# Kernel optimization log

Measured on AMD Instinct MI355X. Metric: run time of the kernel, lower is better.

The kernel has to match this reference:

```python
import jax, jax.numpy as jnp
import numpy as np

N, E, F_IN, H, MH, C, G = 100000, 3200000, 128, 32, 64, 10, 64

def _seg_sum(data, ids, num):
    return jax.ops.segment_sum(data, ids, num_segments=num)

def gcn_conv(x, row, col, ew, W, b, n):
    # PyG GCNConv: linear first, then self-loops + symmetric edge-weight norm + scatter-add
    h = x @ W  # [N, H]
    loop = jnp.arange(n)
    r = jnp.concatenate([row, loop])
    c = jnp.concatenate([col, loop])
    w = jnp.concatenate([ew, jnp.ones((n,), dtype=ew.dtype)])
    deg = _seg_sum(w, c, n)
    dinv = jnp.where(deg > 0, jax.lax.rsqrt(deg), 0.0)
    norm = dinv[r] * w * dinv[c]  # [E+N]
    out = _seg_sum(norm[:, None] * h[r], c, n)  # scatter to targets
    return out + b

def setup_inputs():
    key = jax.random.key(0)
    ks = jax.random.split(key, 16)
    inp = {
        "x": jax.random.normal(ks[0], (N, F_IN), dtype=jnp.float32),
        "edge_index": jax.random.randint(ks[1], (2, E), 0, N, dtype=jnp.int64),
        "edge_weight": jax.random.uniform(ks[2], (E,), dtype=jnp.float32),
        "batch": jnp.sort(jax.random.randint(ks[3], (N,), 0, G, dtype=jnp.int64)),
    }
    def lin(k, i, o):
        s = 1.0 / np.sqrt(i)
        k1, k2 = jax.random.split(k)
        return (jax.random.uniform(k1, (i, o), minval=-s, maxval=s, dtype=jnp.float32),
                jax.random.uniform(k2, (o,), minval=-s, maxval=s, dtype=jnp.float32))
    inp["W1"], inp["b1"] = lin(ks[4], F_IN, H)
    inp["W2"], inp["b2"] = lin(ks[5], H, H)
    inp["W3"], inp["b3"] = lin(ks[6], H, H)
    inp["Wm0"], inp["bm0"] = lin(ks[7], H, MH)
    inp["Wm1"], inp["bm1"] = lin(ks[8], MH, MH)
    inp["Wout"], inp["bout"] = lin(ks[9], MH, C)
    return inp

def reference(x, edge_index, edge_weight, batch, W1, b1, W2, b2, W3, b3, Wm0, bm0, Wm1, bm1, Wout, bout):
    row, col = edge_index[0], edge_index[1]
    h = jax.nn.relu(gcn_conv(x, row, col, edge_weight, W1, b1, N))
    h = jax.nn.relu(gcn_conv(h, row, col, edge_weight, W2, b2, N))
    h = gcn_conv(h, row, col, edge_weight, W3, b3, N)
    # global mean pool over graphs
    sums = _seg_sum(h, batch, G)
    counts = _seg_sum(jnp.ones((N,), dtype=h.dtype), batch, G)
    g = sums / jnp.maximum(counts, 1.0)[:, None]
    # dropout p=0.5 is identity at inference (training=False)
    g = jax.nn.relu(g @ Wm0 + bm0)
    g = jax.nn.relu(g @ Wm1 + bm1)
    return g @ Wout + bout
```

## Files before the change

### kernel.cpp

```cpp
#include <hip/hip_runtime.h>

#define NN 100000
#define NE 3200000
#define FIN 128
#define HID 32
#define MH  64
#define NC  10
#define NG  64
#define NBKT 782
#define NBLK 512
#define EPB  (NE / NBLK)
#define SCANL (NBKT * NBLK)
#define SRCMASK 0x1FFFF
#define BCAP 5120

typedef float floatx2 __attribute__((ext_vector_type(2)));

__global__ __launch_bounds__(1024)
void hist_bkt(const int* __restrict__ ei, int* __restrict__ cnt2) {
    __shared__ int h[NBKT];
    int tid = threadIdx.x, blk = blockIdx.x;
    for (int b = tid; b < NBKT; b += 1024) h[b] = 0;
    __syncthreads();
    int base = blk * EPB;
    for (int i = tid; i < EPB; i += 1024)
        atomicAdd(&h[ei[NE + base + i] >> 7], 1);
    __syncthreads();
    for (int b = tid; b < NBKT; b += 1024) cnt2[blk * NBKT + b] = h[b];
}

__global__ void scan_cnt(const int* __restrict__ cnt2, int* __restrict__ out,
                         int* __restrict__ bsum) {
    __shared__ int lds[256];
    int tid = threadIdx.x;
    int base = blockIdx.x * 1024 + tid * 4;
    int g0 = base, g1 = base + 1, g2 = base + 2, g3 = base + 3;
    int v0 = cnt2[(g0 & (NBLK - 1)) * NBKT + (g0 >> 9)];
    int v1 = cnt2[(g1 & (NBLK - 1)) * NBKT + (g1 >> 9)];
    int v2 = cnt2[(g2 & (NBLK - 1)) * NBKT + (g2 >> 9)];
    int v3 = cnt2[(g3 & (NBLK - 1)) * NBKT + (g3 >> 9)];
    int s = v0 + v1 + v2 + v3;
    lds[tid] = s;
    __syncthreads();
    for (int off = 1; off < 256; off <<= 1) {
        int val = (tid >= off) ? lds[tid - off] : 0;
        __syncthreads();
        lds[tid] += val;
        __syncthreads();
    }
    int excl = lds[tid] - s;
    if (tid == 255) bsum[blockIdx.x] = lds[255];
    out[base + 0] = excl;
    out[base + 1] = excl + v0;
    out[base + 2] = excl + v0 + v1;
    out[base + 3] = excl + v0 + v1 + v2;
}

__global__ void scan_top(int* __restrict__ bsum, int nb, float* __restrict__ sc) {
    int lane = threadIdx.x;
    for (int i = lane; i < NG * HID + NG; i += 64) sc[i] = 0.0f;
    int carry = 0;
    for (int base = 0; base < nb; base += 64) {
        int i = base + lane;
        int orig = (i < nb) ? bsum[i] : 0;
        int v = orig;
#pragma unroll
        for (int off = 1; off < 64; off <<= 1) {
            int t = __shfl_up(v, off, 64);
            if (lane >= off) v += t;
        }
        if (i < nb) bsum[i] = carry + v - orig;
        carry += __shfl(v, 63, 64);
    }
}

__global__ __launch_bounds__(1024)
void scatter_bkt(const int* __restrict__ ei, const float* __restrict__ ew,
                 const int* __restrict__ cnt2, const int* __restrict__ scanned,
                 const int* __restrict__ bsum, int2* __restrict__ tre) {
    __shared__ int2 pay[EPB];
    __shared__ int scur[NBKT];
    __shared__ int hexc[NBKT];
    __shared__ int gbase[NBKT];
    int tid = threadIdx.x, blk = blockIdx.x;
    int myh = 0;
    if (tid < NBKT) {
        int idx = tid * NBLK + blk;
        myh = cnt2[blk * NBKT + tid];
        gbase[tid] = scanned[idx] + bsum[idx >> 10];
        scur[tid] = myh;
    }
    __syncthreads();
    for (int off = 1; off < NBKT; off <<= 1) {
        int v = (tid < NBKT && tid >= off) ? scur[tid - off] : 0;
        __syncthreads();
        if (tid < NBKT) scur[tid] += v;
        __syncthreads();
    }
    if (tid < NBKT) { int ex = scur[tid] - myh; hexc[tid] = ex; scur[tid] = ex; }
    __syncthreads();
    int base = blk * EPB;
    for (int i = tid; i < EPB; i += 1024) {
        int e = base + i;
        int c = ei[NE + e];
        int r = ei[e];
        unsigned int wb = __float_as_uint(ew[e]);
        int b = c >> 7;
        int j = atomicAdd(&scur[b], 1);
        pay[j] = make_int2(r | ((c & 127) << 17) | ((b & 0xFF) << 24),
                           (int)((wb & ~3u) | ((unsigned)b >> 8)));
    }
    __syncthreads();
    for (int j = tid; j < EPB; j += 1024) {
        int2 q = pay[j];
        int b = (int)((((unsigned)q.y & 3u) << 8) | (((unsigned)q.x >> 24) & 0xFFu));
        int pos = gbase[b] + (j - hexc[b]);
        tre[pos] = make_int2(q.x & 0x00FFFFFF, q.y & ~3);
    }
}

__global__ __launch_bounds__(512)
void sort_k(const int2* __restrict__ tre, const int* __restrict__ scanned,
            const int* __restrict__ bsum, unsigned int* __restrict__ srn4,
            int* __restrict__ rowptr, float* __restrict__ dinv) {
    __shared__ int2 ed[BCAP];
    __shared__ int h[128];
    __shared__ float dw[128];
    __shared__ int cur[128];
    int b = blockIdx.x, tid = threadIdx.x;
    int base = scanned[b * NBLK] + bsum[(b * NBLK) >> 10];
    int end = (b == NBKT - 1)
                  ? NE
                  : scanned[(b + 1) * NBLK] + bsum[((b + 1) * NBLK) >> 10];
    int n = end - base;
    bool staged = (n <= BCAP);
    if (tid < 128) { h[tid] = 0; dw[tid] = 0.f; }
    __syncthreads();
    for (int i = tid; i < n; i += 512) {
        int2 q = tre[base + i];
        if (staged) ed[i] = q;
        int key = (q.x >> 17) & 127;
        atomicAdd(&h[key], 1);
        atomicAdd(&dw[key], __int_as_float(q.y));
    }
    __syncthreads();
    if (tid < 64) {
        int lane = tid;
        int carry = 0;
#pragma unroll
        for (int c = 0; c < 2; ++c) {
            int idx = c * 64 + lane;
            int hv = h[idx];
            int v = hv;
#pragma unroll
            for (int off = 1; off < 64; off <<= 1) {
                int t = __shfl_up(v, off, 64);
                if (lane >= off) v += t;
            }
            cur[idx] = base + carry + v - hv;
            int node = b * 128 + idx;
            if (node < NN) {
                rowptr[node] = base + carry + v;
                dinv[node] = rsqrtf(1.0f + dw[idx]);
            }
            carry += __shfl(v, 63, 64);
        }
    }
    __syncthreads();
    for (int i = tid; i < n; i += 512) {
        int2 q = staged ? ed[i] : tre[base + i];
        int key = (q.x >> 17) & 127;
        int pos = atomicAdd(&cur[key], 1);
        unsigned int wb = (unsigned)q.y;
        wb += 0x7FFFu + ((wb >> 16) & 1u);
        srn4[pos] = (unsigned)(q.x & SRCMASK) | (((wb >> 16) & 0x7FFFu) << 17);
    }
}

template <int IN_DIM, bool RELU_IN>
__global__ __launch_bounds__(256)
void linear_k(const float* __restrict__ in, const float* __restrict__ W,
              const float* __restrict__ dinv, unsigned int* __restrict__ tmp8) {
    constexpr int J4 = IN_DIM / 4;
    constexpr int XSS = J4 + 1;
    __shared__ float4 xs[64 * XSS];
    __shared__ float4 wp[IN_DIM * 8];
    int tid = threadIdx.x;
    for (int idx = tid; idx < IN_DIM * 8; idx += 256) {
        int j = idx >> 3, kg = idx & 7;
        const float* wr = W + j * 32 + kg * 4;
        wp[idx] = make_float4(wr[0], wr[1], wr[2], wr[3]);
    }
    int rbase = blockIdx.x * 64;
    const float4* in4 = (const float4*)in;
    for (int idx = tid; idx < 64 * J4; idx += 256) {
        int row = idx / J4, j4 = idx % J4;
        int grow = rbase + row;
        float4 v = (grow < NN) ? in4[(size_t)grow * J4 + j4]
                               : make_float4(0.f, 0.f, 0.f, 0.f);
        if (RELU_IN) {
            v.x = fmaxf(v.x, 0.f); v.y = fmaxf(v.y, 0.f);
            v.z = fmaxf(v.z, 0.f); v.w = fmaxf(v.w, 0.f);
        }
        xs[row * XSS + j4] = v;
    }
    __syncthreads();
    int kg = tid & 7;
    int rp = tid >> 3;
    int r0 = rbase + 2 * rp;
    if (r0 >= NN) return;
    const float4* x0 = &xs[(2 * rp) * XSS];
    const float4* x1 = &xs[(2 * rp + 1) * XSS];
    float a00 = 0, a01 = 0, a02 = 0, a03 = 0;
    float a10 = 0, a11 = 0, a12 = 0, a13 = 0;
#pragma unroll
    for (int j4 = 0; j4 < J4; ++j4) {
        float4 v0 = x0[j4], v1 = x1[j4];
        const float4* wj = &wp[j4 * 4 * 8 + kg];
        float4 w0 = wj[0], w1 = wj[8], w2 = wj[16], w3 = wj[24];
#define LSTEP(VX0, VX1, W4) \
        a00 = fmaf(VX0, W4.x, a00); a01 = fmaf(VX0, W4.y, a01); \
        a02 = fmaf(VX0, W4.z, a02); a03 = fmaf(VX0, W4.w, a03); \
        a10 = fmaf(VX1, W4.x, a10); a11 = fmaf(VX1, W4.y, a11); \
        a12 = fmaf(VX1, W4.z, a12); a13 = fmaf(VX1, W4.w, a13);
        LSTEP(v0.x, v1.x, w0)
        LSTEP(v0.y, v1.y, w1)
        LSTEP(v0.z, v1.z, w2)
        LSTEP(v0.w, v1.w, w3)
#undef LSTEP
    }
    float d0 = dinv[r0], d1 = dinv[r0 + 1];
    a00 *= d0; a01 *= d0; a02 *= d0; a03 *= d0;
    a10 *= d1; a11 *= d1; a12 *= d1; a13 *= d1;
    int q0 = __builtin_amdgcn_cvt_pk_fp8_f32(a00, a01, 0, false);
    q0 = __builtin_amdgcn_cvt_pk_fp8_f32(a02, a03, q0, true);
    int q1 = __builtin_amdgcn_cvt_pk_fp8_f32(a10, a11, 0, false);
    q1 = __builtin_amdgcn_cvt_pk_fp8_f32(a12, a13, q1, true);
    tmp8[r0 * 8 + kg] = (unsigned int)q0;
    tmp8[(r0 + 1) * 8 + kg] = (unsigned int)q1;
}

struct AccR { floatx2 r0, r1, r2, r3, r4, r5, r6, r7; };

#define ACC8(A0,A1,A2,A3,A4,A5,A6,A7, U, W) { \
    floatx2 lo_, hi_; \
    lo_ = __builtin_amdgcn_cvt_pk_f32_fp8(U.x, false); \
    hi_ = __builtin_amdgcn_cvt_pk_f32_fp8(U.x, true); \
    A0 += lo_ * W; A1 += hi_ * W; \
    lo_ = __builtin_amdgcn_cvt_pk_f32_fp8(U.y, false); \
    hi_ = __builtin_amdgcn_cvt_pk_f32_fp8(U.y, true); \
    A2 += lo_ * W; A3 += hi_ * W; \
    lo_ = __builtin_amdgcn_cvt_pk_f32_fp8(U.z, false); \
    hi_ = __builtin_amdgcn_cvt_pk_f32_fp8(U.z, true); \
    A4 += lo_ * W; A5 += hi_ * W; \
    lo_ = __builtin_amdgcn_cvt_pk_f32_fp8(U.w, false); \
    hi_ = __builtin_amdgcn_cvt_pk_f32_fp8(U.w, true); \
    A6 += lo_ * W; A7 += hi_ * W; }

__device__ __forceinline__ AccR agg_core(const unsigned int* __restrict__ srn4,
                                         const int* __restrict__ rowptr,
                                         const unsigned int* __restrict__ tmp8,
                                         int nid, int s, unsigned int cb) {
    const char* t8 = (const char*)tmp8;
    int end = rowptr[nid];
    int start = (nid == 0) ? 0 : rowptr[nid - 1];
    floatx2 a0 = {0.f,0.f}, a1 = {0.f,0.f}, a2 = {0.f,0.f}, a3 = {0.f,0.f};
    floatx2 a4 = {0.f,0.f}, a5 = {0.f,0.f}, a6 = {0.f,0.f}, a7 = {0.f,0.f};
    floatx2 b0 = {0.f,0.f}, b1 = {0.f,0.f}, b2 = {0.f,0.f}, b3 = {0.f,0.f};
    floatx2 b4 = {0.f,0.f}, b5 = {0.f,0.f}, b6 = {0.f,0.f}, b7 = {0.f,0.f};
    int eM = end - 1;
    for (int e = start + s; e < end; e += 32) {
        int i1 = min(e + 8, eM);
        int i2 = min(e + 16, eM);
        int i3 = min(e + 24, eM);
        unsigned int p0 = srn4[e];
        unsigned int p1 = srn4[i1];
        unsigned int p2 = srn4[i2];
        unsigned int p3 = srn4[i3];
        uint4 u0 = *(const uint4*)(t8 + (((p0 & SRCMASK) << 5) | cb));
        uint4 u1 = *(const uint4*)(t8 + (((p1 & SRCMASK) << 5) | cb));
        uint4 u2 = *(const uint4*)(t8 + (((p2 & SRCMASK) << 5) | cb));
        uint4 u3 = *(const uint4*)(t8 + (((p3 & SRCMASK) << 5) | cb));
        float w0 = __uint_as_float((p0 >> 1) & 0x7FFF0000u);
        float w1 = (e + 8  <= eM) ? __uint_as_float((p1 >> 1) & 0x7FFF0000u) : 0.f;
        float w2 = (e + 16 <= eM) ? __uint_as_float((p2 >> 1) & 0x7FFF0000u) : 0.f;
        float w3 = (e + 24 <= eM) ? __uint_as_float((p3 >> 1) & 0x7FFF0000u) : 0.f;
        ACC8(a0,a1,a2,a3,a4,a5,a6,a7, u0, w0)
        ACC8(b0,b1,b2,b3,b4,b5,b6,b7, u1, w1)
        ACC8(a0,a1,a2,a3,a4,a5,a6,a7, u2, w2)
        ACC8(b0,b1,b2,b3,b4,b5,b6,b7, u3, w3)
    }
    a0 += b0; a1 += b1; a2 += b2; a3 += b3;
    a4 += b4; a5 += b5; a6 += b6; a7 += b7;
#define REDM(M) { \
    a0.x += __shfl_xor(a0.x, M, 64); a0.y += __shfl_xor(a0.y, M, 64); \
    a1.x += __shfl_xor(a1.x, M, 64); a1.y += __shfl_xor(a1.y, M, 64); \
    a2.x += __shfl_xor(a2.x, M, 64); a2.y += __shfl_xor(a2.y, M, 64); \
    a3.x += __shfl_xor(a3.x, M, 64); a3.y += __shfl_xor(a3.y, M, 64); \
    a4.x += __shfl_xor(a4.x, M, 64); a4.y += __shfl_xor(a4.y, M, 64); \
    a5.x += __shfl_xor(a5.x, M, 64); a5.y += __shfl_xor(a5.y, M, 64); \
    a6.x += __shfl_xor(a6.x, M, 64); a6.y += __shfl_xor(a6.y, M, 64); \
    a7.x += __shfl_xor(a7.x, M, 64); a7.y += __shfl_xor(a7.y, M, 64); }
    REDM(2) REDM(4) REDM(8)
#undef REDM
    AccR r;
    r.r0 = a0; r.r1 = a1; r.r2 = a2; r.r3 = a3;
    r.r4 = a4; r.r5 = a5; r.r6 = a6; r.r7 = a7;
    return r;
}

#define EPILOGUE16(O0,O1,O2,O3, NID, CB, D, BIAS, A, RELU) { \
    const char* t8_ = (const char*)tmp8; \
    uint4 sv_ = *(const uint4*)(t8_ + (((unsigned)(NID)) << 5) + (CB)); \
    floatx2 s0_ = __builtin_amdgcn_cvt_pk_f32_fp8(sv_.x, false); \
    floatx2 s1_ = __builtin_amdgcn_cvt_pk_f32_fp8(sv_.x, true); \
    floatx2 s2_ = __builtin_amdgcn_cvt_pk_f32_fp8(sv_.y, false); \
    floatx2 s3_ = __builtin_amdgcn_cvt_pk_f32_fp8(sv_.y, true); \
    floatx2 s4_ = __builtin_amdgcn_cvt_pk_f32_fp8(sv_.z, false); \
    floatx2 s5_ = __builtin_amdgcn_cvt_pk_f32_fp8(sv_.z, true); \
    floatx2 s6_ = __builtin_amdgcn_cvt_pk_f32_fp8(sv_.w, false); \
    floatx2 s7_ = __builtin_amdgcn_cvt_pk_f32_fp8(sv_.w, true); \
    const float4* bp_ = (const float4*)(BIAS) + 4 * c; \
    float4 bq0_ = bp_[0], bq1_ = bp_[1], bq2_ = bp_[2], bq3_ = bp_[3]; \
    O0.x = bq0_.x + (D) * (s0_.x + A.r0.x); \
    O0.y = bq0_.y + (D) * (s0_.y + A.r0.y); \
    O0.z = bq0_.z + (D) * (s1_.x + A.r1.x); \
    O0.w = bq0_.w + (D) * (s1_.y + A.r1.y); \
    O1.x = bq1_.x + (D) * (s2_.x + A.r2.x); \
    O1.y = bq1_.y + (D) * (s2_.y + A.r2.y); \
    O1.z = bq1_.z + (D) * (s3_.x + A.r3.x); \
    O1.w = bq1_.w + (D) * (s3_.y + A.r3.y); \
    O2.x = bq2_.x + (D) * (s4_.x + A.r4.x); \
    O2.y = bq2_.y + (D) * (s4_.y + A.r4.y); \
    O2.z = bq2_.z + (D) * (s5_.x + A.r5.x); \
    O2.w = bq2_.w + (D) * (s5_.y + A.r5.y); \
    O3.x = bq3_.x + (D) * (s6_.x + A.r6.x); \
    O3.y = bq3_.y + (D) * (s6_.y + A.r6.y); \
    O3.z = bq3_.z + (D) * (s7_.x + A.r7.x); \
    O3.w = bq3_.w + (D) * (s7_.y + A.r7.y); \
    if (RELU) { \
        O0.x = fmaxf(O0.x, 0.f); O0.y = fmaxf(O0.y, 0.f); \
        O0.z = fmaxf(O0.z, 0.f); O0.w = fmaxf(O0.w, 0.f); \
        O1.x = fmaxf(O1.x, 0.f); O1.y = fmaxf(O1.y, 0.f); \
        O1.z = fmaxf(O1.z, 0.f); O1.w = fmaxf(O1.w, 0.f); \
        O2.x = fmaxf(O2.x, 0.f); O2.y = fmaxf(O2.y, 0.f); \
        O2.z = fmaxf(O2.z, 0.f); O2.w = fmaxf(O2.w, 0.f); \
        O3.x = fmaxf(O3.x, 0.f); O3.y = fmaxf(O3.y, 0.f); \
        O3.z = fmaxf(O3.z, 0.f); O3.w = fmaxf(O3.w, 0.f); \
    } }

__global__ __launch_bounds__(256)
void aggregate(const unsigned int* __restrict__ srn4,
               const int* __restrict__ rowptr,
               const float* __restrict__ dinv,
               const float* __restrict__ bias,
               const unsigned int* __restrict__ tmp8,
               float* __restrict__ h) {
    int tid = threadIdx.x;
    int nid = (blockIdx.x * 256 + tid) >> 4;
    int lane = tid & 63;
    int c = lane & 1, s = (lane >> 1) & 7;
    unsigned int cb = (unsigned int)c * 16u;
    AccR A = agg_core(srn4, rowptr, tmp8, nid, s, cb);
    if ((lane & 14) == 0) {
        float d = dinv[nid];
        float4 o0, o1, o2, o3;
        EPILOGUE16(o0, o1, o2, o3, nid, cb, d, bias, A, false)
        float4* hp = (float4*)(h + (size_t)nid * HID + 16 * c);
        hp[0] = o0; hp[1] = o1; hp[2] = o2; hp[3] = o3;
    }
}

__global__ __launch_bounds__(256)
void agg_lin(const unsigned int* __restrict__ srn4,
             const int* __restrict__ rowptr,
             const float* __restrict__ dinv,
             const float* __restrict__ bias,
             const float* __restrict__ Wn,
             const unsigned int* __restrict__ tmp8,
             unsigned int* __restrict__ tmp8_out) {
    __shared__ float hrow[4][4][HID];
    __shared__ float Wt[32][36];
    int tid = threadIdx.x;
    for (int idx = tid; idx < 1024; idx += 256)
        Wt[idx & 31][idx >> 5] = Wn[idx];
    int nid = (blockIdx.x * 256 + tid) >> 4;
    int wv = tid >> 6;
    int lane = tid & 63;
    int n = (lane >> 4) & 3;
    int c = lane & 1, s = (lane >> 1) & 7;
    unsigned int cb = (unsigned int)c * 16u;
    __syncthreads();
    AccR A = agg_core(srn4, rowptr, tmp8, nid, s, cb);
    float d = dinv[nid];
    if ((lane & 14) == 0) {
        float4 o0, o1, o2, o3;
        EPILOGUE16(o0, o1, o2, o3, nid, cb, d, bias, A, true)
        float4* hp = (float4*)&hrow[wv][n][16 * c];
        hp[0] = o0; hp[1] = o1; hp[2] = o2; hp[3] = o3;
    }
    int j0 = lane & 15;
    const float4* hb = (const float4*)&hrow[wv][n][0];
    float4 h0 = hb[0], h1 = hb[1], h2 = hb[2], h3 = hb[3];
    float4 h4 = hb[4], h5 = hb[5], h6 = hb[6], h7 = hb[7];
    const float4* w0p = (const float4*)&Wt[j0][0];
    const float4* w1p = (const float4*)&Wt[j0 + 16][0];
    float y0 = 0.f, y1 = 0.f;
#define MVSTEP(K, HV) { float4 wa_ = w0p[K]; float4 wb_ = w1p[K]; \
    y0 = fmaf(HV.x, wa_.x, y0); y0 = fmaf(HV.y, wa_.y, y0); \
    y0 = fmaf(HV.z, wa_.z, y0); y0 = fmaf(HV.w, wa_.w, y0); \
    y1 = fmaf(HV.x, wb_.x, y1); y1 = fmaf(HV.y, wb_.y, y1); \
    y1 = fmaf(HV.z, wb_.z, y1); y1 = fmaf(HV.w, wb_.w, y1); }
    MVSTEP(0, h0) MVSTEP(1, h1) MVSTEP(2, h2) MVSTEP(3, h3)
    MVSTEP(4, h4) MVSTEP(5, h5) MVSTEP(6, h6) MVSTEP(7, h7)
#undef MVSTEP
    y0 *= d; y1 *= d;
    float p1 = __shfl_down(y0, 1, 64);
    float p2 = __shfl_down(y0, 2, 64);
    float p3 = __shfl_down(y0, 3, 64);
    float q1 = __shfl_down(y1, 1, 64);
    float q2 = __shfl_down(y1, 2, 64);
    float q3 = __shfl_down(y1, 3, 64);
    if ((j0 & 3) == 0) {
        int t = j0 >> 2;
        int w0 = __builtin_amdgcn_cvt_pk_fp8_f32(y0, p1, 0, false);
        w0 = __builtin_amdgcn_cvt_pk_fp8_f32(p2, p3, w0, true);
        int w1 = __builtin_amdgcn_cvt_pk_fp8_f32(y1, q1, 0, false);
        w1 = __builtin_amdgcn_cvt_pk_fp8_f32(q2, q3, w1, true);
        tmp8_out[nid * 8 + t] = (unsigned int)w0;
        tmp8_out[nid * 8 + 4 + t] = (unsigned int)w1;
    }
}

__global__ void pool_k(const float* __restrict__ h, const int* __restrict__ batch,
                       float* __restrict__ sums, float* __restrict__ counts) {
    int t = blockIdx.x * 256 + threadIdx.x;
    int chunk = t >> 5, k = t & 31;
    int n0 = chunk * 32;
    if (n0 >= NN) return;
    int n1 = min(n0 + 32, NN);
    int g = batch[n0];
    float acc = 0.f, cacc = 0.f;
    for (int i = n0; i < n1; ++i) {
        int gi = batch[i];
        if (gi != g) {
            atomicAdd(&sums[g * HID + k], acc);
            if (k == 0) atomicAdd(&counts[g], cacc);
            g = gi; acc = 0.f; cacc = 0.f;
        }
        acc += h[(size_t)i * HID + k];
        cacc += 1.f;
    }
    atomicAdd(&sums[g * HID + k], acc);
    if (k == 0) atomicAdd(&counts[g], cacc);
}

__global__ __launch_bounds__(64)
void mlp_k(const float* __restrict__ sums, const float* __restrict__ counts,
           const float* __restrict__ Wm0, const float* __restrict__ bm0,
           const float* __restrict__ Wm1, const float* __restrict__ bm1,
           const float* __restrict__ Wout, const float* __restrict__ bout,
           float* __restrict__ out) {
    __shared__ float g0[HID];
    __shared__ float g1[MH];
    __shared__ float g2[MH];
    int g = blockIdx.x;
    int k = threadIdx.x;
    if (k < HID) g0[k] = sums[g * HID + k] / fmaxf(counts[g], 1.0f);
    __syncthreads();
    float acc = bm0[k];
#pragma unroll
    for (int j = 0; j < HID; ++j) acc = fmaf(g0[j], Wm0[j * MH + k], acc);
    g1[k] = fmaxf(acc, 0.f);
    __syncthreads();
    float acc2 = bm1[k];
#pragma unroll
    for (int j = 0; j < MH; ++j) acc2 = fmaf(g1[j], Wm1[j * MH + k], acc2);
    g2[k] = fmaxf(acc2, 0.f);
    __syncthreads();
    if (k < NC) {
        float acc3 = bout[k];
#pragma unroll
        for (int j = 0; j < MH; ++j) acc3 = fmaf(g2[j], Wout[j * NC + k], acc3);
        out[g * NC + k] = acc3;
    }
}

extern "C" void kernel_launch(void* const* d_in, const int* in_sizes, int n_in,
                              void* d_out, int out_size, void* d_ws, size_t ws_size,
                              hipStream_t stream) {
    const float* x    = (const float*)d_in[0];
    const int*   ei   = (const int*)d_in[1];
    const float* ew   = (const float*)d_in[2];
    const int*   batch= (const int*)d_in[3];
    const float* W1   = (const float*)d_in[4];
    const float* b1   = (const float*)d_in[5];
    const float* W2   = (const float*)d_in[6];
    const float* b2   = (const float*)d_in[7];
    const float* W3   = (const float*)d_in[8];
    const float* b3   = (const float*)d_in[9];
    const float* Wm0  = (const float*)d_in[10];
    const float* bm0  = (const float*)d_in[11];
    const float* Wm1  = (const float*)d_in[12];
    const float* bm1  = (const float*)d_in[13];
    const float* Wout = (const float*)d_in[14];
    const float* bout = (const float*)d_in[15];
    float* out = (float*)d_out;

    char* p = (char*)d_ws;
    unsigned int* srn4 = (unsigned int*)p; p += sizeof(unsigned int) * (size_t)NE;
    char*  S   = p;                      p += 12 * (size_t)NE;
    int2*  tre = (int2*)S;
    int*   cnt2    = (int*)(S + sizeof(int2) * (size_t)NE);
    int*   scanned = cnt2 + SCANL;
    unsigned int* tmp8  = (unsigned int*)S;
    unsigned int* tmp8b = tmp8 + (size_t)NN * 8;
    float* hA  = (float*)(S + 2 * (size_t)NN * HID);
    int*   bsum    = (int*)p;            p += sizeof(int) * 512;
    float* dinv    = (float*)p;          p += sizeof(float) * NN;
    int*   rowptr  = (int*)p;            p += sizeof(int) * NN;
    float* sums    = (float*)p;          p += sizeof(float) * NG * HID;
    float* counts  = (float*)p;

    dim3 blk(256);
    const int NB_SCAN = (SCANL + 1023) / 1024;
    const int NB_LIN = (NN + 63) / 64;
    const int NB_AGG = 6250;

    hist_bkt<<<NBLK, 1024, 0, stream>>>(ei, cnt2);
    scan_cnt<<<NB_SCAN, blk, 0, stream>>>(cnt2, scanned, bsum);
    scan_top<<<1, 64, 0, stream>>>(bsum, NB_SCAN, sums);
    scatter_bkt<<<NBLK, 1024, 0, stream>>>(ei, ew, cnt2, scanned, bsum, tre);
    sort_k<<<NBKT, 512, 0, stream>>>(tre, scanned, bsum, srn4, rowptr, dinv);

    linear_k<FIN, false><<<NB_LIN, blk, 0, stream>>>(x, W1, dinv, tmp8);
    agg_lin<<<NB_AGG, blk, 0, stream>>>(srn4, rowptr, dinv, b1, W2, tmp8, tmp8b);
    agg_lin<<<NB_AGG, blk, 0, stream>>>(srn4, rowptr, dinv, b2, W3, tmp8b, tmp8);
    aggregate<<<NB_AGG, blk, 0, stream>>>(srn4, rowptr, dinv, b3, tmp8, hA);

    pool_k<<<391, blk, 0, stream>>>(hA, batch, sums, counts);
    mlp_k<<<NG, 64, 0, stream>>>(sums, counts, Wm0, bm0, Wm1, bm1, Wout, bout, out);
}
```

Measured before the change: 355.4 us.

## Fuse top-level scan into scan kernel, split sort histograms, store final features as bf16

The single-block top-level scan is folded into the scan kernel through a last-block-done atomic counter, which removes one kernel launch. The sort kernel now uses two LDS histogram copies, one per 256-thread half, to reduce atomic contention. The final aggregation writes bf16-packed features instead of fp32, and pooling reads and unpacks them to halve that traffic. The trade-off is lower precision in the pooled features and added reliance on threadfence/atomic ordering for the fused scan.

```diff
diff --git a/kernel.cpp b/kernel.cpp
--- a/kernel.cpp
+++ b/kernel.cpp
@@ -11,15 +11,24 @@
 #define NBLK 512
 #define EPB  (NE / NBLK)
 #define SCANL (NBKT * NBLK)
+#define NB_SCAN 391
 #define SRCMASK 0x1FFFF
 #define BCAP 5120
 
 typedef float floatx2 __attribute__((ext_vector_type(2)));
 
+__device__ __forceinline__ unsigned int pkbf(float a, float b) {
+    unsigned ua = __float_as_uint(a); ua += 0x7FFFu + ((ua >> 16) & 1u);
+    unsigned ub = __float_as_uint(b); ub += 0x7FFFu + ((ub >> 16) & 1u);
+    return (ua >> 16) | (ub & 0xFFFF0000u);
+}
+
 __global__ __launch_bounds__(1024)
-void hist_bkt(const int* __restrict__ ei, int* __restrict__ cnt2) {
+void hist_bkt(const int* __restrict__ ei, int* __restrict__ cnt2,
+              int* __restrict__ bsum) {
     __shared__ int h[NBKT];
     int tid = threadIdx.x, blk = blockIdx.x;
+    if (blk == 0 && tid == 0) bsum[500] = 0;
     for (int b = tid; b < NBKT; b += 1024) h[b] = 0;
     __syncthreads();
     int base = blk * EPB;
@@ -29,9 +38,10 @@
     for (int b = tid; b < NBKT; b += 1024) cnt2[blk * NBKT + b] = h[b];
 }
 
-__global__ void scan_cnt(const int* __restrict__ cnt2, int* __restrict__ out,
-                         int* __restrict__ bsum) {
+__global__ void scan_k(const int* __restrict__ cnt2, int* __restrict__ out,
+                       int* __restrict__ bsum, float* __restrict__ sc) {
     __shared__ int lds[256];
+    __shared__ int amLast;
     int tid = threadIdx.x;
     int base = blockIdx.x * 1024 + tid * 4;
     int g0 = base, g1 = base + 1, g2 = base + 2, g3 = base + 3;
@@ -49,28 +59,37 @@
         __syncthreads();
     }
     int excl = lds[tid] - s;
-    if (tid == 255) bsum[blockIdx.x] = lds[255];
+    if (tid == 255) {
+        bsum[blockIdx.x] = lds[255];
+        __threadfence();
+    }
     out[base + 0] = excl;
     out[base + 1] = excl + v0;
     out[base + 2] = excl + v0 + v1;
     out[base + 3] = excl + v0 + v1 + v2;
-}
-
-__global__ void scan_top(int* __restrict__ bsum, int nb, float* __restrict__ sc) {
-    int lane = threadIdx.x;
-    for (int i = lane; i < NG * HID + NG; i += 64) sc[i] = 0.0f;
-    int carry = 0;
-    for (int base = 0; base < nb; base += 64) {
-        int i = base + lane;
-        int orig = (i < nb) ? bsum[i] : 0;
-        int v = orig;
-#pragma unroll
-        for (int off = 1; off < 64; off <<= 1) {
-            int t = __shfl_up(v, off, 64);
-            if (lane >= off) v += t;
+    __syncthreads();
+    if (tid == 0) {
+        int t = atomicAdd(&bsum[500], 1);
+        amLast = (t == NB_SCAN - 1);
+    }
+    __syncthreads();
+    if (!amLast) return;
+    for (int i = tid; i < NG * HID + NG; i += 256) sc[i] = 0.0f;
+    if (tid < 64) {
+        int lane = tid;
+        int carry = 0;
+        for (int b0 = 0; b0 < NB_SCAN; b0 += 64) {
+            int i = b0 + lane;
+            int orig = (i < NB_SCAN) ? atomicAdd(&bsum[i], 0) : 0;
+            int v = orig;
+#pragma unroll
+            for (int off = 1; off < 64; off <<= 1) {
+                int t2 = __shfl_up(v, off, 64);
+                if (lane >= off) v += t2;
+            }
+            if (i < NB_SCAN) bsum[i] = carry + v - orig;
+            carry += __shfl(v, 63, 64);
         }
-        if (i < nb) bsum[i] = carry + v - orig;
-        carry += __shfl(v, 63, 64);
     }
 }
 
@@ -124,8 +143,8 @@
             const int* __restrict__ bsum, unsigned int* __restrict__ srn4,
             int* __restrict__ rowptr, float* __restrict__ dinv) {
     __shared__ int2 ed[BCAP];
-    __shared__ int h[128];
-    __shared__ float dw[128];
+    __shared__ int h2[2][128];
+    __shared__ float dw2[2][128];
     __shared__ int cur[128];
     int b = blockIdx.x, tid = threadIdx.x;
     int base = scanned[b * NBLK] + bsum[(b * NBLK) >> 10];
@@ -134,14 +153,18 @@
                   : scanned[(b + 1) * NBLK] + bsum[((b + 1) * NBLK) >> 10];
     int n = end - base;
     bool staged = (n <= BCAP);
-    if (tid < 128) { h[tid] = 0; dw[tid] = 0.f; }
-    __syncthreads();
+    if (tid < 128) {
+        h2[0][tid] = 0; h2[1][tid] = 0;
+        dw2[0][tid] = 0.f; dw2[1][tid] = 0.f;
+    }
+    __syncthreads();
+    int grp = tid >> 8;
     for (int i = tid; i < n; i += 512) {
         int2 q = tre[base + i];
         if (staged) ed[i] = q;
         int key = (q.x >> 17) & 127;
-        atomicAdd(&h[key], 1);
-        atomicAdd(&dw[key], __int_as_float(q.y));
+        atomicAdd(&h2[grp][key], 1);
+        atomicAdd(&dw2[grp][key], __int_as_float(q.y));
     }
     __syncthreads();
     if (tid < 64) {
@@ -150,7 +173,7 @@
 #pragma unroll
         for (int c = 0; c < 2; ++c) {
             int idx = c * 64 + lane;
-            int hv = h[idx];
+            int hv = h2[0][idx] + h2[1][idx];
             int v = hv;
 #pragma unroll
             for (int off = 1; off < 64; off <<= 1) {
@@ -161,7 +184,7 @@
             int node = b * 128 + idx;
             if (node < NN) {
                 rowptr[node] = base + carry + v;
-                dinv[node] = rsqrtf(1.0f + dw[idx]);
+                dinv[node] = rsqrtf(1.0f + dw2[0][idx] + dw2[1][idx]);
             }
             carry += __shfl(v, 63, 64);
         }
@@ -355,7 +378,7 @@
                const float* __restrict__ dinv,
                const float* __restrict__ bias,
                const unsigned int* __restrict__ tmp8,
-               float* __restrict__ h) {
+               unsigned int* __restrict__ hb) {
     int tid = threadIdx.x;
     int nid = (blockIdx.x * 256 + tid) >> 4;
     int lane = tid & 63;
@@ -366,8 +389,13 @@
         float d = dinv[nid];
         float4 o0, o1, o2, o3;
         EPILOGUE16(o0, o1, o2, o3, nid, cb, d, bias, A, false)
-        float4* hp = (float4*)(h + (size_t)nid * HID + 16 * c);
-        hp[0] = o0; hp[1] = o1; hp[2] = o2; hp[3] = o3;
+        uint4 w0, w1;
+        w0.x = pkbf(o0.x, o0.y); w0.y = pkbf(o0.z, o0.w);
+        w0.z = pkbf(o1.x, o1.y); w0.w = pkbf(o1.z, o1.w);
+        w1.x = pkbf(o2.x, o2.y); w1.y = pkbf(o2.z, o2.w);
+        w1.z = pkbf(o3.x, o3.y); w1.w = pkbf(o3.z, o3.w);
+        uint4* hp = (uint4*)(hb + (size_t)nid * 16 + 8 * c);
+        hp[0] = w0; hp[1] = w1;
     }
 }
 
@@ -432,13 +460,15 @@
     }
 }
 
-__global__ void pool_k(const float* __restrict__ h, const int* __restrict__ batch,
+__global__ void pool_k(const unsigned int* __restrict__ hb,
+                       const int* __restrict__ batch,
                        float* __restrict__ sums, float* __restrict__ counts) {
     int t = blockIdx.x * 256 + threadIdx.x;
     int chunk = t >> 5, k = t & 31;
     int n0 = chunk * 32;
     if (n0 >= NN) return;
     int n1 = min(n0 + 32, NN);
+    int j = k >> 1, odd = k & 1;
     int g = batch[n0];
     float acc = 0.f, cacc = 0.f;
     for (int i = n0; i < n1; ++i) {
@@ -448,7 +478,9 @@
             if (k == 0) atomicAdd(&counts[g], cacc);
             g = gi; acc = 0.f; cacc = 0.f;
         }
-        acc += h[(size_t)i * HID + k];
+        unsigned int w = hb[(size_t)i * 16 + j];
+        unsigned int bits = odd ? (w & 0xFFFF0000u) : (w << 16);
+        acc += __uint_as_float(bits);
         cacc += 1.f;
     }
     atomicAdd(&sums[g * HID + k], acc);
@@ -515,7 +547,7 @@
     int*   scanned = cnt2 + SCANL;
     unsigned int* tmp8  = (unsigned int*)S;
     unsigned int* tmp8b = tmp8 + (size_t)NN * 8;
-    float* hA  = (float*)(S + 2 * (size_t)NN * HID);
+    unsigned int* hb = (unsigned int*)(S + 2 * (size_t)NN * HID);
     int*   bsum    = (int*)p;            p += sizeof(int) * 512;
     float* dinv    = (float*)p;          p += sizeof(float) * NN;
     int*   rowptr  = (int*)p;            p += sizeof(int) * NN;
@@ -523,21 +555,19 @@
     float* counts  = (float*)p;
 
     dim3 blk(256);
-    const int NB_SCAN = (SCANL + 1023) / 1024;
     const int NB_LIN = (NN + 63) / 64;
     const int NB_AGG = 6250;
 
-    hist_bkt<<<NBLK, 1024, 0, stream>>>(ei, cnt2);
-    scan_cnt<<<NB_SCAN, blk, 0, stream>>>(cnt2, scanned, bsum);
-    scan_top<<<1, 64, 0, stream>>>(bsum, NB_SCAN, sums);
+    hist_bkt<<<NBLK, 1024, 0, stream>>>(ei, cnt2, bsum);
+    scan_k<<<NB_SCAN, blk, 0, stream>>>(cnt2, scanned, bsum, sums);
     scatter_bkt<<<NBLK, 1024, 0, stream>>>(ei, ew, cnt2, scanned, bsum, tre);
     sort_k<<<NBKT, 512, 0, stream>>>(tre, scanned, bsum, srn4, rowptr, dinv);
 
     linear_k<FIN, false><<<NB_LIN, blk, 0, stream>>>(x, W1, dinv, tmp8);
     agg_lin<<<NB_AGG, blk, 0, stream>>>(srn4, rowptr, dinv, b1, W2, tmp8, tmp8b);
     agg_lin<<<NB_AGG, blk, 0, stream>>>(srn4, rowptr, dinv, b2, W3, tmp8b, tmp8);
-    aggregate<<<NB_AGG, blk, 0, stream>>>(srn4, rowptr, dinv, b3, tmp8, hA);
-
-    pool_k<<<391, blk, 0, stream>>>(hA, batch, sums, counts);
+    aggregate<<<NB_AGG, blk, 0, stream>>>(srn4, rowptr, dinv, b3, tmp8, hb);
+
+    pool_k<<<391, blk, 0, stream>>>(hb, batch, sums, counts);
     mlp_k<<<NG, 64, 0, stream>>>(sums, counts, Wm0, bm0, Wm1, bm1, Wout, bout, out);
 }
```

After: 362.9 us. 2.1% more time.
